# Optimization experiments

Measured on AMD Instinct MI355X. Metric: run time of the kernel, lower is better.

Reference implementation:

```python
import jax, jax.numpy as jnp
import numpy as np

D_MODEL = 1024
NUM_HEADS = 16
D_K = D_MODEL // NUM_HEADS


def setup_inputs() -> dict:
    key = jax.random.key(0)
    ks = jax.random.split(key, 7)
    B, S = 2, 2048
    query = jax.random.normal(ks[0], (B, S, D_MODEL), dtype=jnp.float32)
    key_t = jax.random.normal(ks[1], (B, S, D_MODEL), dtype=jnp.float32)
    value = jax.random.normal(ks[2], (B, S, D_MODEL), dtype=jnp.float32)
    attention_mask = jnp.ones((B, S), dtype=jnp.int32)
    # xavier_uniform for square d_model x d_model: limit = sqrt(6/(fan_in+fan_out))
    limit = np.sqrt(6.0 / (D_MODEL + D_MODEL)).astype(np.float32)
    def xav(k):
        return jax.random.uniform(k, (D_MODEL, D_MODEL), dtype=jnp.float32, minval=-limit, maxval=limit)
    return {
        "query": query, "key": key_t, "value": value,
        "attention_mask": attention_mask,
        "w_q": xav(ks[3]), "w_k": xav(ks[4]), "w_v": xav(ks[5]), "w_o": xav(ks[6]),
    }


def reference(query, key, value, attention_mask, w_q, w_k, w_v, w_o):
    B, S, _ = query.shape
    # torch Linear: x @ W.T  (weights stored [out, in])
    def proj(x, w):
        y = jnp.einsum('bsd,ed->bse', x, w)
        return y.reshape(B, S, NUM_HEADS, D_K).transpose(0, 2, 1, 3)  # [B,H,S,Dk]
    q = proj(query, w_q)
    k = proj(key, w_k)
    v = proj(value, w_v)
    scores = jnp.einsum('bhqd,bhkd->bhqk', q, k) / jnp.sqrt(jnp.float32(D_K))
    # mask [B,S] -> [B,1,1,S]; masked_fill where mask == 0
    mask = (attention_mask[:, None, None, :] == 0)
    scores = jnp.where(mask, jnp.float32(-1e9), scores)
    attn = jax.nn.softmax(scores, axis=-1)
    # dropout p=0.0 (eval) -> identity
    context = jnp.einsum('bhqk,bhkd->bhqd', attn, v)
    context = context.transpose(0, 2, 1, 3).reshape(B, S, D_MODEL)
    return jnp.einsum('bsd,ed->bse', context, w_o)
```

## Files before the change

### kernel.cpp

```cpp
#include <hip/hip_runtime.h>
#include <hip/hip_bf16.h>


typedef short short8  __attribute__((ext_vector_type(8)));
typedef short short4v __attribute__((ext_vector_type(4)));
typedef float f32x4   __attribute__((ext_vector_type(4)));

#define D_MODEL 1024
#define SEQ     2048
#define NHEAD   16
#define DKD     64
#define HSTR    (SEQ * DKD)
#define QSCALE  0.1803368801111204f
#define EXP2F(x) exp2f(x)

#define MFMA16(a, b, c) __builtin_amdgcn_mfma_f32_16x16x32_bf16((a), (b), (c), 0, 0, 0)

__device__ __forceinline__ ushort f2bf(float f) {
    __hip_bfloat16 h = __float2bfloat16(f);
    return __builtin_bit_cast(ushort, h);
}

__device__ __forceinline__ short8 frag128(const ushort* base, int row, int c0) {
    int cb = (c0 * 2) ^ ((row & 7) << 4);
    return *(const short8*)((const char*)base + row * 128 + cb);
}
__device__ __forceinline__ short8 frag256(const ushort* base, int row, int c0) {
    int cb = (c0 * 2) ^ ((row & 7) << 4);
    return *(const short8*)((const char*)base + row * 256 + cb);
}

__global__ __launch_bounds__(256) void cvt_w(
    const float* __restrict__ s0, const float* __restrict__ s1, const float* __restrict__ s2,
    ushort* __restrict__ dst)
{
    const int z = blockIdx.y;
    const float* s = (z == 0) ? s0 : ((z == 1) ? s1 : s2);
    ushort* d = dst + (size_t)z * 1048576;
    const int i = (blockIdx.x * 256 + threadIdx.x) * 8;
    f32x4 a = *(const f32x4*)(s + i);
    f32x4 b = *(const f32x4*)(s + i + 4);
    short8 o;
    #pragma unroll
    for (int u = 0; u < 4; ++u) { o[u] = (short)f2bf(a[u]); o[4 + u] = (short)f2bf(b[u]); }
    *(short8*)(d + i) = o;
}

template<int LAYOUT, int A_BF16>
__global__ __launch_bounds__(256, 3) void gemm_nt(
    const void* __restrict__ A0, const void* __restrict__ A1, const void* __restrict__ A2,
    const ushort* __restrict__ W0, const ushort* __restrict__ W1, const ushort* __restrict__ W2,
    void* __restrict__ O0, void* __restrict__ O1, void* __restrict__ O2)
{
    const int z = blockIdx.z;
    const void*   A = (z == 0) ? A0 : ((z == 1) ? A1 : A2);
    const ushort* W = (z == 0) ? W0 : ((z == 1) ? W1 : W2);
    void* O         = (z == 0) ? O0 : ((z == 1) ? O1 : O2);

    const int bm = blockIdx.x * 128;
    const int bn = blockIdx.y * 128;
    const int tid = threadIdx.x;
    const int w = tid >> 6, l = tid & 63;
    const int wr = w >> 1, wc = w & 1;

    __shared__ ushort sm[16384];

    f32x4 acc[4][4] = {};
    short8 areg[4], wreg[4];
    const int srow = tid >> 3;
    const int sc8  = (tid & 7) << 3;
    const int scb  = (sc8 * 2);

    #define GLOADT(t_) {                                                                    \
        _Pragma("unroll")                                                                   \
        for (int i = 0; i < 4; ++i) {                                                       \
            int row = i * 32 + srow;                                                        \
            if (A_BF16) {                                                                   \
                areg[i] = *(const short8*)((const ushort*)A + (size_t)(bm + row) * 1024 + (t_) * 64 + sc8); \
            } else {                                                                        \
                const float* ap = (const float*)A + (size_t)(bm + row) * 1024 + (t_) * 64 + sc8; \
                f32x4 x0 = *(const f32x4*)ap, x1 = *(const f32x4*)(ap + 4);                 \
                _Pragma("unroll")                                                           \
                for (int u = 0; u < 4; ++u) { areg[i][u] = (short)f2bf(x0[u]); areg[i][4 + u] = (short)f2bf(x1[u]); } \
            }                                                                               \
            wreg[i] = *(const short8*)(W + (size_t)(bn + row) * 1024 + (t_) * 64 + sc8);    \
        } }

    #define GWRITET() {                                                                     \
        _Pragma("unroll")                                                                   \
        for (int i = 0; i < 4; ++i) {                                                       \
            int row = i * 32 + srow;                                                        \
            int cb  = scb ^ ((row & 7) << 4);                                               \
            *(short8*)((char*)sm + row * 128 + cb) = areg[i];                               \
            *(short8*)((char*)(sm + 8192) + row * 128 + cb) = wreg[i];                      \
        } }

    GLOADT(0);
    #pragma unroll 1
    for (int t = 0; t < 16; ++t) {
        GWRITET();
        __syncthreads();
        if (t < 15) GLOADT(t + 1);

        #pragma unroll
        for (int kk = 0; kk < 2; ++kk) {
            const int c0 = kk * 32 + ((l >> 4) << 3);
            short8 af[4], bf[4];
            #pragma unroll
            for (int mi = 0; mi < 4; ++mi)
                af[mi] = frag128(sm, wr * 64 + mi * 16 + (l & 15), c0);
            #pragma unroll
            for (int ni = 0; ni < 4; ++ni)
                bf[ni] = frag128(sm + 8192, wc * 64 + ni * 16 + (l & 15), c0);
            #pragma unroll
            for (int mi = 0; mi < 4; ++mi)
                #pragma unroll
                for (int ni = 0; ni < 4; ++ni)
                    acc[mi][ni] = MFMA16(af[mi], bf[ni], acc[mi][ni]);
        }
        __syncthreads();
    }
    #undef GLOADT
    #undef GWRITET

    if (LAYOUT == 0 && z == 2) {
        #pragma unroll
        for (int mi = 0; mi < 4; ++mi) {
            #pragma unroll
            for (int ni = 0; ni < 4; ++ni) {
                int n_l = wc * 64 + ni * 16 + (l & 15);
                int m0  = wr * 64 + mi * 16 + ((l >> 4) << 2);
                short4v v4;
                #pragma unroll
                for (int j = 0; j < 4; ++j) v4[j] = (short)f2bf(acc[mi][ni][j]);
                *(short4v*)((char*)sm + n_l * 256 + ((m0 * 2) ^ ((n_l & 7) << 4))) = v4;
            }
        }
        __syncthreads();
        const int row = tid >> 1, half = tid & 1;
        const int n_g = bn + row;
        const int bb  = bm >> 11;
        ushort* Op = (ushort*)O + (size_t)(bb * NHEAD + (n_g >> 6)) * HSTR
                     + (size_t)(n_g & 63) * SEQ + (bm & 2047) + half * 64;
        #pragma unroll
        for (int u = 0; u < 8; ++u) {
            short8 c = *(const short8*)((char*)sm + row * 256
                        + (((half * 64 + u * 8) * 2) ^ ((row & 7) << 4)));
            *(short8*)(Op + u * 8) = c;
        }
        return;
    }

    const float sc = (LAYOUT == 0 && z == 0) ? QSCALE : 1.0f;
    #pragma unroll
    for (int mi = 0; mi < 4; ++mi) {
        #pragma unroll
        for (int ni = 0; ni < 4; ++ni) {
            #pragma unroll
            for (int j = 0; j < 4; ++j) {
                int m = bm + wr * 64 + mi * 16 + ((l >> 4) << 2) + j;
                int n = bn + wc * 64 + ni * 16 + (l & 15);
                if (LAYOUT == 0) {
                    int b = m >> 11, s = m & 2047, h = n >> 6, dk = n & 63;
                    ((ushort*)O)[(size_t)(b * NHEAD + h) * HSTR + s * DKD + dk] = f2bf(acc[mi][ni][j] * sc);
                } else {
                    ((float*)O)[(size_t)m * 1024 + n] = acc[mi][ni][j];
                }
            }
        }
    }
}

__global__ __launch_bounds__(512, 4) void attn_fwd(
    const ushort* __restrict__ Q, const ushort* __restrict__ K, const ushort* __restrict__ Vt,
    const int* __restrict__ mask, ushort* __restrict__ ctx)
{
    const int tid = threadIdx.x;
    const int w = tid >> 6, l = tid & 63;
    const int hi = l >> 4, lo = l & 15;
    const int id  = blockIdx.x;
    const int nid = (id & 7) * 64 + (id >> 3);
    const int bh  = nid >> 4;
    const int q0  = (nid & 15) * 128;
    const int b   = bh >> 4, h = bh & 15;

    __shared__ ushort sm[2][16384];
    __shared__ int mflag;

    if (tid == 0) mflag = 1;
    __syncthreads();
    {
        int4 m0 = ((const int4*)(mask + b * SEQ))[tid];
        if (!(m0.x && m0.y && m0.z && m0.w)) mflag = 0;
    }

    const ushort* Qh = Q  + (size_t)bh * HSTR;
    const ushort* Kh = K  + (size_t)bh * HSTR;
    const ushort* Vh = Vt + (size_t)bh * HSTR;

    short8 qf[2];
    #pragma unroll
    for (int kk = 0; kk < 2; ++kk)
        qf[kk] = *(const short8*)(Qh + (size_t)(q0 + w * 16 + lo) * DKD + kk * 32 + hi * 8);

    f32x4 acc_o[4] = {};
    float m_run = -INFINITY, l_run = 0.0f;

    const int kr = tid >> 3;
    const int kc = (tid & 7) << 3;
    const int vr = tid >> 4;
    const int vkpb = (tid & 15) << 4;

    short8  kreg[2];
    short4v vreg0[2], vreg1[2];

    #define LOADT(kt_) {                                                                   \
        _Pragma("unroll")                                                                  \
        for (int i = 0; i < 2; ++i)                                                        \
            kreg[i] = *(const short8*)(Kh + (size_t)((kt_) * 128 + i * 64 + kr) * DKD + kc); \
        _Pragma("unroll")                                                                  \
        for (int i = 0; i < 2; ++i) {                                                      \
            const ushort* vp = Vh + (size_t)(i * 32 + vr) * SEQ + (kt_) * 128 + ((tid >> 2) & 3) * 32 + (tid & 3) * 4; \
            vreg0[i] = *(const short4v*)(vp);                                              \
            vreg1[i] = *(const short4v*)(vp + 16); } }

    #define WRITET(buf_) {                                                                 \
        _Pragma("unroll")                                                                  \
        for (int i = 0; i < 2; ++i) {                                                      \
            int r = i * 64 + kr;                                                           \
            *(short8*)((char*)sm[buf_] + r * 128 + ((kc * 2) ^ ((r & 7) << 4))) = kreg[i]; } \
        _Pragma("unroll")                                                                  \
        for (int i = 0; i < 2; ++i) {                                                      \
            int r = i * 32 + vr;                                                           \
            char* p = (char*)(sm[buf_] + 8192) + r * 256 + (vkpb ^ ((r & 7) << 4));        \
            *(short4v*)(p)     = vreg0[i];                                                 \
            *(short4v*)(p + 8) = vreg1[i]; } }

    LOADT(0); WRITET(0);
    __syncthreads();
    const bool allones = (mflag != 0);
    const f32x4 zf = {};

    #define HALF(nb_) {                                                                    \
        f32x4* s = s4 + 4 * (nb_);                                                         \
        if (!allones) {                                                                    \
            const int* mrow = mask + b * SEQ + kt * 128 + (nb_) * 64 + hi * 4;             \
            _Pragma("unroll")                                                              \
            for (int ni = 0; ni < 4; ++ni) {                                               \
                int4 mv = *(const int4*)(mrow + ni * 16);                                  \
                s[ni][0] = mv.x ? s[ni][0] : -1e9f;                                        \
                s[ni][1] = mv.y ? s[ni][1] : -1e9f;                                        \
                s[ni][2] = mv.z ? s[ni][2] : -1e9f;                                        \
                s[ni][3] = mv.w ? s[ni][3] : -1e9f;                                        \
            }                                                                              \
        }                                                                                  \
        float t0 = fmaxf(fmaxf(s[0][0], s[0][1]), fmaxf(s[0][2], s[0][3]));                \
        float t1 = fmaxf(fmaxf(s[1][0], s[1][1]), fmaxf(s[1][2], s[1][3]));                \
        float t2 = fmaxf(fmaxf(s[2][0], s[2][1]), fmaxf(s[2][2], s[2][3]));                \
        float t3 = fmaxf(fmaxf(s[3][0], s[3][1]), fmaxf(s[3][2], s[3][3]));                \
        float t = fmaxf(fmaxf(t0, t1), fmaxf(t2, t3));                                     \
        t = fmaxf(t, __shfl_xor(t, 16));                                                   \
        t = fmaxf(t, __shfl_xor(t, 32));                                                   \
        if (!__all(t <= m_run + 8.0f)) {       \
            float mnew = fmaxf(m_run, t);                                                  \
            float c = EXP2F(m_run - mnew);                                                 \
            m_run = mnew;                                                                  \
            l_run *= c;                                                                    \
            float cj[4];                                                                   \
            _Pragma("unroll")                                                              \
            for (int j = 0; j < 4; ++j) cj[j] = __shfl(c, (l & 48) | (hi * 4 + j));        \
            _Pragma("unroll")                                                              \
            for (int ni = 0; ni < 4; ++ni)                                                 \
                _Pragma("unroll")                                                          \
                for (int j = 0; j < 4; ++j) acc_o[ni][j] *= cj[j];                         \
        }                                                                                  \
        float rsA = 0.0f;                                                                  \
        _Pragma("unroll")                                                                  \
        for (int ni = 0; ni < 4; ++ni) {                                                   \
            _Pragma("unroll")                                                              \
            for (int j = 0; j < 4; ++j) s[ni][j] = EXP2F(s[ni][j] - m_run);                \
            rsA += (s[ni][0] + s[ni][1]) + (s[ni][2] + s[ni][3]);                          \
        }                                                                                  \
        rsA += __shfl_xor(rsA, 16);                                                        \
        rsA += __shfl_xor(rsA, 32);                                                        \
        l_run += rsA;                                                                      \
        short8 pa[2];                                                                      \
        _Pragma("unroll")                                                                  \
        for (int kk = 0; kk < 2; ++kk) {                                                   \
            _Pragma("unroll")                                                              \
            for (int j = 0; j < 4; ++j) {                                                  \
                pa[kk][j]     = (short)f2bf(s[2 * kk][j]);                                 \
                pa[kk][4 + j] = (short)f2bf(s[2 * kk + 1][j]);                             \
            }                                                                              \
        }                                                                                  \
        __builtin_amdgcn_s_setprio(1);                                                     \
        _Pragma("unroll")                                                                  \
        for (int kk = 0; kk < 2; ++kk) {                                                   \
            const int c0 = ((nb_) * 2 + kk) * 32 + hi * 8;                                 \
            _Pragma("unroll")                                                              \
            for (int ni = 0; ni < 4; ++ni) {                                               \
                short8 vf = frag256(vb, ni * 16 + lo, c0);                                 \
                acc_o[ni] = MFMA16(pa[kk], vf, acc_o[ni]);                                 \
            }                                                                              \
        }                                                                                  \
        __builtin_amdgcn_s_setprio(0); }

    #pragma unroll 1
    for (int kt = 0; kt < 16; ++kt) {
        const int cur = kt & 1;
        const ushort* kb = sm[cur];
        const ushort* vb = sm[cur] + 8192;

        if (kt < 15) LOADT(kt + 1);

        f32x4 s4[8];
        __builtin_amdgcn_s_setprio(1);
        #pragma unroll
        for (int ni = 0; ni < 8; ++ni)
            s4[ni] = MFMA16(frag128(kb, ni * 16 + lo, hi * 8), qf[0], zf);
        #pragma unroll
        for (int ni = 0; ni < 8; ++ni)
            s4[ni] = MFMA16(frag128(kb, ni * 16 + lo, 32 + hi * 8), qf[1], s4[ni]);
        __builtin_amdgcn_s_setprio(0);

        HALF(0)
        if (kt < 15) WRITET(cur ^ 1);
        HALF(1)

        __syncthreads();
    }
    #undef HALF
    #undef LOADT
    #undef WRITET

    float inv = 1.0f / l_run;
    float invj[4];
    #pragma unroll
    for (int j = 0; j < 4; ++j)
        invj[j] = __shfl(inv, (l & 48) | (hi * 4 + j));
    #pragma unroll
    for (int ni = 0; ni < 4; ++ni)
        #pragma unroll
        for (int j = 0; j < 4; ++j) {
            int qg = q0 + w * 16 + hi * 4 + j;
            ctx[(size_t)(b * SEQ + qg) * D_MODEL + h * DKD + ni * 16 + lo] = f2bf(acc_o[ni][j] * invj[j]);
        }
}

__global__ void ws_sentinel(float* __restrict__ out, int n, float code) {
    int i = blockIdx.x * blockDim.x + threadIdx.x;
    if (i < n) out[i] = (i == 0) ? code : 0.0f;
}

extern "C" void kernel_launch(void* const* d_in, const int* in_sizes, int n_in,
                              void* d_out, int out_size, void* d_ws, size_t ws_size,
                              hipStream_t stream) {
    const float* q    = (const float*)d_in[0];
    const float* k    = (const float*)d_in[1];
    const float* v    = (const float*)d_in[2];
    const int*   mask = (const int*)d_in[3];
    const float* wq   = (const float*)d_in[4];
    const float* wk   = (const float*)d_in[5];
    const float* wv   = (const float*)d_in[6];
    const float* wo   = (const float*)d_in[7];
    float* out = (float*)d_out;

    if (ws_size < (size_t)33554432) {
        float code = 100.0f + (float)(ws_size >> 20);
        ws_sentinel<<<(out_size + 255) / 256, 256, 0, stream>>>(out, out_size, code);
        return;
    }

    ushort* ws = (ushort*)d_ws;
    ushort* Qb = ws;
    ushort* Kb = ws + 4194304;
    ushort* Vb = ws + 8388608;
    ushort* Cb = ws + 12582912;

    dim3 blk(256, 1, 1);
    cvt_w<<<dim3(512, 3), blk, 0, stream>>>(wq, wk, wv, Cb);
    gemm_nt<0, 0><<<dim3(32, 8, 3), blk, 0, stream>>>(
        q, k, v, Cb, Cb + 1048576, Cb + 2097152, Qb, Kb, Vb);
    attn_fwd<<<dim3(512, 1, 1), dim3(512, 1, 1), 0, stream>>>(Qb, Kb, Vb, mask, Cb);
    cvt_w<<<dim3(512, 1), blk, 0, stream>>>(wo, wo, wo, Qb);
    gemm_nt<1, 1><<<dim3(32, 8, 1), blk, 0, stream>>>(
        Cb, Cb, Cb, Qb, Qb, Qb, out, out, out);
}
```

Measured before the change: 136.2 us.

## Switch attention to 32x32 MFMA with split-KV wave groups and LDS merge

Rewrites the attention inner loop to use 32x32x16 bf16 MFMA tiles instead of 16x16x32. Each wave now owns 32 query rows, and the two wave groups each process half of every 128-key tile. The two partial softmax states are combined at the end through shared memory. The goal is to cut LDS fragment reads and issue overhead per MFMA, and to halve per-wave softmax work per tile, at the cost of an extra final merge, more accumulator registers, and a changed V staging layout.

```diff
diff --git a/kernel.cpp b/kernel.cpp
--- a/kernel.cpp
+++ b/kernel.cpp
@@ -5,6 +5,7 @@
 typedef short short8  __attribute__((ext_vector_type(8)));
 typedef short short4v __attribute__((ext_vector_type(4)));
 typedef float f32x4   __attribute__((ext_vector_type(4)));
+typedef float f32x16  __attribute__((ext_vector_type(16)));
 
 #define D_MODEL 1024
 #define SEQ     2048
@@ -15,6 +16,7 @@
 #define EXP2F(x) exp2f(x)
 
 #define MFMA16(a, b, c) __builtin_amdgcn_mfma_f32_16x16x32_bf16((a), (b), (c), 0, 0, 0)
+#define MFMA32(a, b, c) __builtin_amdgcn_mfma_f32_32x32x16_bf16((a), (b), (c), 0, 0, 0)
 
 __device__ __forceinline__ ushort f2bf(float f) {
     __hip_bfloat16 h = __float2bfloat16(f);
@@ -177,7 +179,8 @@
 {
     const int tid = threadIdx.x;
     const int w = tid >> 6, l = tid & 63;
-    const int hi = l >> 4, lo = l & 15;
+    const int l31 = l & 31, hi5 = l >> 5;
+    const int g = w >> 2, wq = w & 3;
     const int id  = blockIdx.x;
     const int nid = (id & 7) * 64 + (id >> 3);
     const int bh  = nid >> 4;
@@ -198,112 +201,43 @@
     const ushort* Kh = K  + (size_t)bh * HSTR;
     const ushort* Vh = Vt + (size_t)bh * HSTR;
 
-    short8 qf[2];
+    short8 qf[4];
     #pragma unroll
-    for (int kk = 0; kk < 2; ++kk)
-        qf[kk] = *(const short8*)(Qh + (size_t)(q0 + w * 16 + lo) * DKD + kk * 32 + hi * 8);
-
-    f32x4 acc_o[4] = {};
+    for (int kk = 0; kk < 4; ++kk)
+        qf[kk] = *(const short8*)(Qh + (size_t)(q0 + wq * 32 + l31) * DKD + kk * 16 + hi5 * 8);
+
+    f32x16 acc0 = {}, acc1 = {};
     float m_run = -INFINITY, l_run = 0.0f;
 
-    const int kr = tid >> 3;
-    const int kc = (tid & 7) << 3;
-    const int vr = tid >> 4;
-    const int vkpb = (tid & 15) << 4;
-
+    const int kr  = tid >> 3;
+    const int oct = tid & 7;
+    const int vq  = oct & 3, vhalf = oct >> 2;
+    const int kcb = oct << 4;
     short8  kreg[2];
-    short4v vreg0[2], vreg1[2];
+    short4v vreg[4];
 
     #define LOADT(kt_) {                                                                   \
-        _Pragma("unroll")                                                                  \
-        for (int i = 0; i < 2; ++i)                                                        \
-            kreg[i] = *(const short8*)(Kh + (size_t)((kt_) * 128 + i * 64 + kr) * DKD + kc); \
-        _Pragma("unroll")                                                                  \
-        for (int i = 0; i < 2; ++i) {                                                      \
-            const ushort* vp = Vh + (size_t)(i * 32 + vr) * SEQ + (kt_) * 128 + ((tid >> 2) & 3) * 32 + (tid & 3) * 4; \
-            vreg0[i] = *(const short4v*)(vp);                                              \
-            vreg1[i] = *(const short4v*)(vp + 16); } }
+        kreg[0] = *(const short8*)(Kh + (size_t)((kt_) * 128 + kr) * DKD + (oct << 3));    \
+        kreg[1] = *(const short8*)(Kh + (size_t)((kt_) * 128 + 64 + kr) * DKD + (oct << 3)); \
+        const ushort* vp = Vh + (size_t)kr * SEQ + (kt_) * 128 + vhalf * 64 + vq * 16;     \
+        vreg[0] = *(const short4v*)(vp);                                                   \
+        vreg[1] = *(const short4v*)(vp + 8);                                               \
+        vreg[2] = *(const short4v*)(vp + 4);                                               \
+        vreg[3] = *(const short4v*)(vp + 12); }
 
     #define WRITET(buf_) {                                                                 \
-        _Pragma("unroll")                                                                  \
-        for (int i = 0; i < 2; ++i) {                                                      \
-            int r = i * 64 + kr;                                                           \
-            *(short8*)((char*)sm[buf_] + r * 128 + ((kc * 2) ^ ((r & 7) << 4))) = kreg[i]; } \
-        _Pragma("unroll")                                                                  \
-        for (int i = 0; i < 2; ++i) {                                                      \
-            int r = i * 32 + vr;                                                           \
-            char* p = (char*)(sm[buf_] + 8192) + r * 256 + (vkpb ^ ((r & 7) << 4));        \
-            *(short4v*)(p)     = vreg0[i];                                                 \
-            *(short4v*)(p + 8) = vreg1[i]; } }
+        { int r = kr;      *(short8*)((char*)sm[buf_] + r * 128 + (kcb ^ ((r & 7) << 4))) = kreg[0]; } \
+        { int r = 64 + kr; *(short8*)((char*)sm[buf_] + r * 128 + (kcb ^ ((r & 7) << 4))) = kreg[1]; } \
+        { char* p = (char*)(sm[buf_] + 8192) + kr * 256;                                   \
+          int pb = (vhalf * 64 + vq * 16) * 2;                                             \
+          _Pragma("unroll")                                                                \
+          for (int u = 0; u < 4; ++u)                                                      \
+            *(short4v*)(p + ((pb + 8 * u) ^ ((kr & 7) << 4))) = vreg[u]; } }
 
     LOADT(0); WRITET(0);
     __syncthreads();
     const bool allones = (mflag != 0);
-    const f32x4 zf = {};
-
-    #define HALF(nb_) {                                                                    \
-        f32x4* s = s4 + 4 * (nb_);                                                         \
-        if (!allones) {                                                                    \
-            const int* mrow = mask + b * SEQ + kt * 128 + (nb_) * 64 + hi * 4;             \
-            _Pragma("unroll")                                                              \
-            for (int ni = 0; ni < 4; ++ni) {                                               \
-                int4 mv = *(const int4*)(mrow + ni * 16);                                  \
-                s[ni][0] = mv.x ? s[ni][0] : -1e9f;                                        \
-                s[ni][1] = mv.y ? s[ni][1] : -1e9f;                                        \
-                s[ni][2] = mv.z ? s[ni][2] : -1e9f;                                        \
-                s[ni][3] = mv.w ? s[ni][3] : -1e9f;                                        \
-            }                                                                              \
-        }                                                                                  \
-        float t0 = fmaxf(fmaxf(s[0][0], s[0][1]), fmaxf(s[0][2], s[0][3]));                \
-        float t1 = fmaxf(fmaxf(s[1][0], s[1][1]), fmaxf(s[1][2], s[1][3]));                \
-        float t2 = fmaxf(fmaxf(s[2][0], s[2][1]), fmaxf(s[2][2], s[2][3]));                \
-        float t3 = fmaxf(fmaxf(s[3][0], s[3][1]), fmaxf(s[3][2], s[3][3]));                \
-        float t = fmaxf(fmaxf(t0, t1), fmaxf(t2, t3));                                     \
-        t = fmaxf(t, __shfl_xor(t, 16));                                                   \
-        t = fmaxf(t, __shfl_xor(t, 32));                                                   \
-        if (!__all(t <= m_run + 8.0f)) {       \
-            float mnew = fmaxf(m_run, t);                                                  \
-            float c = EXP2F(m_run - mnew);                                                 \
-            m_run = mnew;                                                                  \
-            l_run *= c;                                                                    \
-            float cj[4];                                                                   \
-            _Pragma("unroll")                                                              \
-            for (int j = 0; j < 4; ++j) cj[j] = __shfl(c, (l & 48) | (hi * 4 + j));        \
-            _Pragma("unroll")                                                              \
-            for (int ni = 0; ni < 4; ++ni)                                                 \
-                _Pragma("unroll")                                                          \
-                for (int j = 0; j < 4; ++j) acc_o[ni][j] *= cj[j];                         \
-        }                                                                                  \
-        float rsA = 0.0f;                                                                  \
-        _Pragma("unroll")                                                                  \
-        for (int ni = 0; ni < 4; ++ni) {                                                   \
-            _Pragma("unroll")                                                              \
-            for (int j = 0; j < 4; ++j) s[ni][j] = EXP2F(s[ni][j] - m_run);                \
-            rsA += (s[ni][0] + s[ni][1]) + (s[ni][2] + s[ni][3]);                          \
-        }                                                                                  \
-        rsA += __shfl_xor(rsA, 16);                                                        \
-        rsA += __shfl_xor(rsA, 32);                                                        \
-        l_run += rsA;                                                                      \
-        short8 pa[2];                                                                      \
-        _Pragma("unroll")                                                                  \
-        for (int kk = 0; kk < 2; ++kk) {                                                   \
-            _Pragma("unroll")                                                              \
-            for (int j = 0; j < 4; ++j) {                                                  \
-                pa[kk][j]     = (short)f2bf(s[2 * kk][j]);                                 \
-                pa[kk][4 + j] = (short)f2bf(s[2 * kk + 1][j]);                             \
-            }                                                                              \
-        }                                                                                  \
-        __builtin_amdgcn_s_setprio(1);                                                     \
-        _Pragma("unroll")                                                                  \
-        for (int kk = 0; kk < 2; ++kk) {                                                   \
-            const int c0 = ((nb_) * 2 + kk) * 32 + hi * 8;                                 \
-            _Pragma("unroll")                                                              \
-            for (int ni = 0; ni < 4; ++ni) {                                               \
-                short8 vf = frag256(vb, ni * 16 + lo, c0);                                 \
-                acc_o[ni] = MFMA16(pa[kk], vf, acc_o[ni]);                                 \
-            }                                                                              \
-        }                                                                                  \
-        __builtin_amdgcn_s_setprio(0); }
+    const f32x16 zf = {};
 
     #pragma unroll 1
     for (int kt = 0; kt < 16; ++kt) {
@@ -313,38 +247,112 @@
 
         if (kt < 15) LOADT(kt + 1);
 
-        f32x4 s4[8];
+        f32x16 s4[2];
         __builtin_amdgcn_s_setprio(1);
         #pragma unroll
-        for (int ni = 0; ni < 8; ++ni)
-            s4[ni] = MFMA16(frag128(kb, ni * 16 + lo, hi * 8), qf[0], zf);
-        #pragma unroll
-        for (int ni = 0; ni < 8; ++ni)
-            s4[ni] = MFMA16(frag128(kb, ni * 16 + lo, 32 + hi * 8), qf[1], s4[ni]);
+        for (int t = 0; t < 2; ++t) {
+            s4[t] = MFMA32(frag128(kb, g * 64 + t * 32 + l31, hi5 * 8), qf[0], zf);
+            #pragma unroll
+            for (int kk = 1; kk < 4; ++kk)
+                s4[t] = MFMA32(frag128(kb, g * 64 + t * 32 + l31, kk * 16 + hi5 * 8), qf[kk], s4[t]);
+        }
         __builtin_amdgcn_s_setprio(0);
 
-        HALF(0)
+        if (!allones) {
+            const int* mrow = mask + b * SEQ + kt * 128 + g * 64 + 4 * hi5;
+            #pragma unroll
+            for (int t = 0; t < 2; ++t)
+                #pragma unroll
+                for (int r4 = 0; r4 < 4; ++r4) {
+                    int4 mv = *(const int4*)(mrow + (t * 4 + r4) * 8);
+                    s4[t][r4 * 4 + 0] = mv.x ? s4[t][r4 * 4 + 0] : -1e9f;
+                    s4[t][r4 * 4 + 1] = mv.y ? s4[t][r4 * 4 + 1] : -1e9f;
+                    s4[t][r4 * 4 + 2] = mv.z ? s4[t][r4 * 4 + 2] : -1e9f;
+                    s4[t][r4 * 4 + 3] = mv.w ? s4[t][r4 * 4 + 3] : -1e9f;
+                }
+        }
+
+        float tm = s4[0][0];
+        #pragma unroll
+        for (int i = 1; i < 16; ++i) tm = fmaxf(tm, s4[0][i]);
+        #pragma unroll
+        for (int i = 0; i < 16; ++i) tm = fmaxf(tm, s4[1][i]);
+        tm = fmaxf(tm, __shfl_xor(tm, 32));
+
+        if (!__all(tm <= m_run + 8.0f)) {
+            float mnew = fmaxf(m_run, tm);
+            float c = EXP2F(m_run - mnew);
+            m_run = mnew;
+            l_run *= c;
+            float cj[16];
+            #pragma unroll
+            for (int r = 0; r < 16; ++r)
+                cj[r] = __shfl(c, (l & 32) | ((r & 3) + 8 * (r >> 2) + 4 * hi5));
+            #pragma unroll
+            for (int r = 0; r < 16; ++r) { acc0[r] *= cj[r]; acc1[r] *= cj[r]; }
+        }
+
+        float rs = 0.0f;
+        #pragma unroll
+        for (int t = 0; t < 2; ++t)
+            #pragma unroll
+            for (int i = 0; i < 16; ++i) { s4[t][i] = EXP2F(s4[t][i] - m_run); rs += s4[t][i]; }
+        rs += __shfl_xor(rs, 32);
+        l_run += rs;
+
+        short8 pa[4];
+        #pragma unroll
+        for (int kk = 0; kk < 4; ++kk)
+            #pragma unroll
+            for (int s = 0; s < 8; ++s)
+                pa[kk][s] = (short)f2bf(s4[kk >> 1][8 * (kk & 1) + s]);
+
         if (kt < 15) WRITET(cur ^ 1);
-        HALF(1)
+
+        __builtin_amdgcn_s_setprio(1);
+        #pragma unroll
+        for (int kk = 0; kk < 4; ++kk) {
+            acc0 = MFMA32(pa[kk], frag256(vb, l31,      g * 64 + kk * 16 + hi5 * 8), acc0);
+            acc1 = MFMA32(pa[kk], frag256(vb, 32 + l31, g * 64 + kk * 16 + hi5 * 8), acc1);
+        }
+        __builtin_amdgcn_s_setprio(0);
 
         __syncthreads();
     }
-    #undef HALF
     #undef LOADT
     #undef WRITET
 
-    float inv = 1.0f / l_run;
-    float invj[4];
-    #pragma unroll
-    for (int j = 0; j < 4; ++j)
-        invj[j] = __shfl(inv, (l & 48) | (hi * 4 + j));
-    #pragma unroll
-    for (int ni = 0; ni < 4; ++ni)
-        #pragma unroll
-        for (int j = 0; j < 4; ++j) {
-            int qg = q0 + w * 16 + hi * 4 + j;
-            ctx[(size_t)(b * SEQ + qg) * D_MODEL + h * DKD + ni * 16 + lo] = f2bf(acc_o[ni][j] * invj[j]);
-        }
+    __syncthreads();
+    float* mls  = (float*)sm;
+    float* accs = (float*)sm + 512;
+    if (g == 1) {
+        float* mp = mls + (wq * 64 + l) * 2;
+        mp[0] = m_run; mp[1] = l_run;
+        float* ap = accs + (wq * 64 + l) * 32;
+        #pragma unroll
+        for (int r = 0; r < 16; ++r) { ap[r] = acc0[r]; ap[16 + r] = acc1[r]; }
+    }
+    __syncthreads();
+    if (g == 0) {
+        const float* mp = mls + (wq * 64 + l) * 2;
+        float mB = mp[0], lB = mp[1];
+        float ms = fmaxf(m_run, mB);
+        float cA = EXP2F(m_run - ms), cB = EXP2F(mB - ms);
+        float li = 1.0f / (cA * l_run + cB * lB);
+        float sA = cA * li, sB = cB * li;
+        const float* ap = accs + (wq * 64 + l) * 32;
+        #pragma unroll
+        for (int r = 0; r < 16; ++r) {
+            int qp = (r & 3) + 8 * (r >> 2) + 4 * hi5;
+            float sAr = __shfl(sA, (l & 32) | qp);
+            float sBr = __shfl(sB, (l & 32) | qp);
+            float v0 = sAr * acc0[r] + sBr * ap[r];
+            float v1 = sAr * acc1[r] + sBr * ap[16 + r];
+            int qg = q0 + wq * 32 + qp;
+            ctx[(size_t)(b * SEQ + qg) * D_MODEL + h * DKD + l31]      = f2bf(v0);
+            ctx[(size_t)(b * SEQ + qg) * D_MODEL + h * DKD + 32 + l31] = f2bf(v1);
+        }
+    }
 }
 
 __global__ void ws_sentinel(float* __restrict__ out, int n, float code) {
```

After: 156.9 us. +15.1%, slower.

## Load GEMM weight tiles directly into LDS with double-buffered global_load_lds

Applied to the files above, without the earlier changes.

The weight operand of the projection GEMM is now loaded straight from global memory into shared memory with global_load_lds, into a double-buffered LDS tile. The source column offset is pre-swizzled so the existing XOR layout is kept. This removes the register staging and LDS write instructions for W and cuts VGPR pressure. In exchange LDS use grows from 32KB to 48KB per block, which may lower occupancy against the launch_bounds target of 3. It also relies on the existing barrier ordering to make the asynchronous LDS writes visible.

```diff
diff --git a/kernel.cpp b/kernel.cpp
--- a/kernel.cpp
+++ b/kernel.cpp
@@ -15,6 +15,10 @@
 #define EXP2F(x) exp2f(x)
 
 #define MFMA16(a, b, c) __builtin_amdgcn_mfma_f32_16x16x32_bf16((a), (b), (c), 0, 0, 0)
+
+#define GLDS16(gp, lp) __builtin_amdgcn_global_load_lds( \
+    (const __attribute__((address_space(1))) void*)(gp), \
+    (__attribute__((address_space(3))) void*)(lp), 16, 0, 0)
 
 __device__ __forceinline__ ushort f2bf(float f) {
     __hip_bfloat16 h = __float2bfloat16(f);
@@ -63,15 +67,16 @@
     const int w = tid >> 6, l = tid & 63;
     const int wr = w >> 1, wc = w & 1;
 
-    __shared__ ushort sm[16384];
+    __shared__ ushort smA[8192];
+    __shared__ ushort smW[2][8192];
 
     f32x4 acc[4][4] = {};
-    short8 areg[4], wreg[4];
+    short8 areg[4];
     const int srow = tid >> 3;
     const int sc8  = (tid & 7) << 3;
     const int scb  = (sc8 * 2);
 
-    #define GLOADT(t_) {                                                                    \
+    #define GLOADA(t_) {                                                                    \
         _Pragma("unroll")                                                                   \
         for (int i = 0; i < 4; ++i) {                                                       \
             int row = i * 32 + srow;                                                        \
@@ -83,35 +88,46 @@
                 _Pragma("unroll")                                                           \
                 for (int u = 0; u < 4; ++u) { areg[i][u] = (short)f2bf(x0[u]); areg[i][4 + u] = (short)f2bf(x1[u]); } \
             }                                                                               \
-            wreg[i] = *(const short8*)(W + (size_t)(bn + row) * 1024 + (t_) * 64 + sc8);    \
         } }
 
-    #define GWRITET() {                                                                     \
+    #define GWRITEA() {                                                                     \
         _Pragma("unroll")                                                                   \
         for (int i = 0; i < 4; ++i) {                                                       \
             int row = i * 32 + srow;                                                        \
             int cb  = scb ^ ((row & 7) << 4);                                               \
-            *(short8*)((char*)sm + row * 128 + cb) = areg[i];                               \
-            *(short8*)((char*)(sm + 8192) + row * 128 + cb) = wreg[i];                      \
+            *(short8*)((char*)smA + row * 128 + cb) = areg[i];                              \
         } }
 
-    GLOADT(0);
+    #define GLDSW(t_, buf_) {                                                               \
+        _Pragma("unroll")                                                                   \
+        for (int i = 0; i < 4; ++i) {                                                       \
+            int flat = i * 256 + tid;                                                       \
+            int row  = flat >> 3;                                                           \
+            int pcb  = (flat & 7) << 4;                                                     \
+            int sc   = (pcb ^ ((row & 7) << 4)) >> 1;                                       \
+            GLDS16(W + (size_t)(bn + row) * 1024 + (t_) * 64 + sc,                          \
+                   &smW[buf_][(i * 4 + w) * 512]);                                          \
+        } }
+
+    GLOADA(0);
+    GLDSW(0, 0);
     #pragma unroll 1
     for (int t = 0; t < 16; ++t) {
-        GWRITET();
+        GWRITEA();
         __syncthreads();
-        if (t < 15) GLOADT(t + 1);
-
+        if (t < 15) { GLOADA(t + 1); GLDSW(t + 1, (t + 1) & 1); }
+
+        const ushort* wb = smW[t & 1];
         #pragma unroll
         for (int kk = 0; kk < 2; ++kk) {
             const int c0 = kk * 32 + ((l >> 4) << 3);
             short8 af[4], bf[4];
             #pragma unroll
             for (int mi = 0; mi < 4; ++mi)
-                af[mi] = frag128(sm, wr * 64 + mi * 16 + (l & 15), c0);
+                af[mi] = frag128(smA, wr * 64 + mi * 16 + (l & 15), c0);
             #pragma unroll
             for (int ni = 0; ni < 4; ++ni)
-                bf[ni] = frag128(sm + 8192, wc * 64 + ni * 16 + (l & 15), c0);
+                bf[ni] = frag128(wb, wc * 64 + ni * 16 + (l & 15), c0);
             #pragma unroll
             for (int mi = 0; mi < 4; ++mi)
                 #pragma unroll
@@ -120,10 +136,12 @@
         }
         __syncthreads();
     }
-    #undef GLOADT
-    #undef GWRITET
+    #undef GLOADA
+    #undef GWRITEA
+    #undef GLDSW
 
     if (LAYOUT == 0 && z == 2) {
+        ushort* tb = &smW[0][0];
         #pragma unroll
         for (int mi = 0; mi < 4; ++mi) {
             #pragma unroll
@@ -133,7 +151,7 @@
                 short4v v4;
                 #pragma unroll
                 for (int j = 0; j < 4; ++j) v4[j] = (short)f2bf(acc[mi][ni][j]);
-                *(short4v*)((char*)sm + n_l * 256 + ((m0 * 2) ^ ((n_l & 7) << 4))) = v4;
+                *(short4v*)((char*)tb + n_l * 256 + ((m0 * 2) ^ ((n_l & 7) << 4))) = v4;
             }
         }
         __syncthreads();
@@ -144,7 +162,7 @@
                      + (size_t)(n_g & 63) * SEQ + (bm & 2047) + half * 64;
         #pragma unroll
         for (int u = 0; u < 8; ++u) {
-            short8 c = *(const short8*)((char*)sm + row * 256
+            short8 c = *(const short8*)((char*)tb + row * 256
                         + (((half * 64 + u * 8) * 2) ^ ((row & 7) << 4)));
             *(short8*)(Op + u * 8) = c;
         }
```

Measured after the change: 139.3 us. 1.02x slower.

## Halve attention block threads so each wave handles two query row groups

Applied to the files above, without the earlier changes.

The attention kernel now runs 256 threads (4 waves) per block instead of 512, and each wave computes 32 query rows as two 16-row groups. Each K fragment and V fragment read from LDS is reused across two MFMAs, which halves the LDS reads per unit of work. The whole 128-key tile is now softmaxed at once rather than in two halves. In exchange, per-thread register use roughly doubles (scores, accumulators, prefetch registers), which can lower occupancy. The global-load work per thread also doubles.

```diff
diff --git a/kernel.cpp b/kernel.cpp
--- a/kernel.cpp
+++ b/kernel.cpp
@@ -171,7 +171,7 @@
     }
 }
 
-__global__ __launch_bounds__(512, 4) void attn_fwd(
+__global__ __launch_bounds__(256, 2) void attn_fwd(
     const ushort* __restrict__ Q, const ushort* __restrict__ K, const ushort* __restrict__ Vt,
     const int* __restrict__ mask, ushort* __restrict__ ctx)
 {
@@ -190,48 +190,52 @@
     if (tid == 0) mflag = 1;
     __syncthreads();
     {
-        int4 m0 = ((const int4*)(mask + b * SEQ))[tid];
-        if (!(m0.x && m0.y && m0.z && m0.w)) mflag = 0;
+        const int4* mp = ((const int4*)(mask + b * SEQ)) + tid;
+        int4 m0 = mp[0], m1 = mp[256];
+        if (!(m0.x && m0.y && m0.z && m0.w && m1.x && m1.y && m1.z && m1.w)) mflag = 0;
     }
 
     const ushort* Qh = Q  + (size_t)bh * HSTR;
     const ushort* Kh = K  + (size_t)bh * HSTR;
     const ushort* Vh = Vt + (size_t)bh * HSTR;
 
-    short8 qf[2];
+    short8 qf[2][2];
     #pragma unroll
-    for (int kk = 0; kk < 2; ++kk)
-        qf[kk] = *(const short8*)(Qh + (size_t)(q0 + w * 16 + lo) * DKD + kk * 32 + hi * 8);
-
-    f32x4 acc_o[4] = {};
-    float m_run = -INFINITY, l_run = 0.0f;
+    for (int g = 0; g < 2; ++g)
+        #pragma unroll
+        for (int kk = 0; kk < 2; ++kk)
+            qf[g][kk] = *(const short8*)(Qh + (size_t)(q0 + w * 32 + g * 16 + lo) * DKD
+                                         + kk * 32 + hi * 8);
+
+    f32x4 acc[2][4] = {};
+    float m_run[2] = {-INFINITY, -INFINITY}, l_run[2] = {0.0f, 0.0f};
 
     const int kr = tid >> 3;
     const int kc = (tid & 7) << 3;
     const int vr = tid >> 4;
     const int vkpb = (tid & 15) << 4;
 
-    short8  kreg[2];
-    short4v vreg0[2], vreg1[2];
+    short8  kreg[4];
+    short4v vreg0[4], vreg1[4];
 
     #define LOADT(kt_) {                                                                   \
         _Pragma("unroll")                                                                  \
-        for (int i = 0; i < 2; ++i)                                                        \
-            kreg[i] = *(const short8*)(Kh + (size_t)((kt_) * 128 + i * 64 + kr) * DKD + kc); \
-        _Pragma("unroll")                                                                  \
-        for (int i = 0; i < 2; ++i) {                                                      \
-            const ushort* vp = Vh + (size_t)(i * 32 + vr) * SEQ + (kt_) * 128 + ((tid >> 2) & 3) * 32 + (tid & 3) * 4; \
+        for (int i = 0; i < 4; ++i)                                                        \
+            kreg[i] = *(const short8*)(Kh + (size_t)((kt_) * 128 + i * 32 + kr) * DKD + kc); \
+        _Pragma("unroll")                                                                  \
+        for (int i = 0; i < 4; ++i) {                                                      \
+            const ushort* vp = Vh + (size_t)(i * 16 + vr) * SEQ + (kt_) * 128 + ((tid >> 2) & 3) * 32 + (tid & 3) * 4; \
             vreg0[i] = *(const short4v*)(vp);                                              \
             vreg1[i] = *(const short4v*)(vp + 16); } }
 
     #define WRITET(buf_) {                                                                 \
         _Pragma("unroll")                                                                  \
-        for (int i = 0; i < 2; ++i) {                                                      \
-            int r = i * 64 + kr;                                                           \
+        for (int i = 0; i < 4; ++i) {                                                      \
+            int r = i * 32 + kr;                                                           \
             *(short8*)((char*)sm[buf_] + r * 128 + ((kc * 2) ^ ((r & 7) << 4))) = kreg[i]; } \
         _Pragma("unroll")                                                                  \
-        for (int i = 0; i < 2; ++i) {                                                      \
-            int r = i * 32 + vr;                                                           \
+        for (int i = 0; i < 4; ++i) {                                                      \
+            int r = i * 16 + vr;                                                           \
             char* p = (char*)(sm[buf_] + 8192) + r * 256 + (vkpb ^ ((r & 7) << 4));        \
             *(short4v*)(p)     = vreg0[i];                                                 \
             *(short4v*)(p + 8) = vreg1[i]; } }
@@ -241,69 +245,57 @@
     const bool allones = (mflag != 0);
     const f32x4 zf = {};
 
-    #define HALF(nb_) {                                                                    \
-        f32x4* s = s4 + 4 * (nb_);                                                         \
+    #define SMG(g_) {                                                                      \
         if (!allones) {                                                                    \
-            const int* mrow = mask + b * SEQ + kt * 128 + (nb_) * 64 + hi * 4;             \
+            const int* mrow = mask + b * SEQ + kt * 128 + hi * 4;                          \
             _Pragma("unroll")                                                              \
-            for (int ni = 0; ni < 4; ++ni) {                                               \
+            for (int ni = 0; ni < 8; ++ni) {                                               \
                 int4 mv = *(const int4*)(mrow + ni * 16);                                  \
-                s[ni][0] = mv.x ? s[ni][0] : -1e9f;                                        \
-                s[ni][1] = mv.y ? s[ni][1] : -1e9f;                                        \
-                s[ni][2] = mv.z ? s[ni][2] : -1e9f;                                        \
-                s[ni][3] = mv.w ? s[ni][3] : -1e9f;                                        \
+                s4[g_][ni][0] = mv.x ? s4[g_][ni][0] : -1e9f;                              \
+                s4[g_][ni][1] = mv.y ? s4[g_][ni][1] : -1e9f;                              \
+                s4[g_][ni][2] = mv.z ? s4[g_][ni][2] : -1e9f;                              \
+                s4[g_][ni][3] = mv.w ? s4[g_][ni][3] : -1e9f;                              \
             }                                                                              \
         }                                                                                  \
-        float t0 = fmaxf(fmaxf(s[0][0], s[0][1]), fmaxf(s[0][2], s[0][3]));                \
-        float t1 = fmaxf(fmaxf(s[1][0], s[1][1]), fmaxf(s[1][2], s[1][3]));                \
-        float t2 = fmaxf(fmaxf(s[2][0], s[2][1]), fmaxf(s[2][2], s[2][3]));                \
-        float t3 = fmaxf(fmaxf(s[3][0], s[3][1]), fmaxf(s[3][2], s[3][3]));                \
-        float t = fmaxf(fmaxf(t0, t1), fmaxf(t2, t3));                                     \
+        float t = fmaxf(fmaxf(s4[g_][0][0], s4[g_][0][1]), fmaxf(s4[g_][0][2], s4[g_][0][3])); \
+        _Pragma("unroll")                                                                  \
+        for (int ni = 1; ni < 8; ++ni) {                                                   \
+            float tn = fmaxf(fmaxf(s4[g_][ni][0], s4[g_][ni][1]),                          \
+                             fmaxf(s4[g_][ni][2], s4[g_][ni][3]));                         \
+            t = fmaxf(t, tn);                                                              \
+        }                                                                                  \
         t = fmaxf(t, __shfl_xor(t, 16));                                                   \
         t = fmaxf(t, __shfl_xor(t, 32));                                                   \
-        if (!__all(t <= m_run + 8.0f)) {       \
-            float mnew = fmaxf(m_run, t);                                                  \
-            float c = EXP2F(m_run - mnew);                                                 \
-            m_run = mnew;                                                                  \
-            l_run *= c;                                                                    \
+        if (!__all(t <= m_run[g_] + 8.0f)) {                                               \
+            float mnew = fmaxf(m_run[g_], t);                                              \
+            float c = EXP2F(m_run[g_] - mnew);                                             \
+            m_run[g_] = mnew;                                                              \
+            l_run[g_] *= c;                                                                \
             float cj[4];                                                                   \
             _Pragma("unroll")                                                              \
             for (int j = 0; j < 4; ++j) cj[j] = __shfl(c, (l & 48) | (hi * 4 + j));        \
             _Pragma("unroll")                                                              \
             for (int ni = 0; ni < 4; ++ni)                                                 \
                 _Pragma("unroll")                                                          \
-                for (int j = 0; j < 4; ++j) acc_o[ni][j] *= cj[j];                         \
+                for (int j = 0; j < 4; ++j) acc[g_][ni][j] *= cj[j];                       \
         }                                                                                  \
-        float rsA = 0.0f;                                                                  \
-        _Pragma("unroll")                                                                  \
-        for (int ni = 0; ni < 4; ++ni) {                                                   \
+        float rs = 0.0f;                                                                   \
+        _Pragma("unroll")                                                                  \
+        for (int ni = 0; ni < 8; ++ni) {                                                   \
             _Pragma("unroll")                                                              \
-            for (int j = 0; j < 4; ++j) s[ni][j] = EXP2F(s[ni][j] - m_run);                \
-            rsA += (s[ni][0] + s[ni][1]) + (s[ni][2] + s[ni][3]);                          \
+            for (int j = 0; j < 4; ++j) s4[g_][ni][j] = EXP2F(s4[g_][ni][j] - m_run[g_]);  \
+            rs += (s4[g_][ni][0] + s4[g_][ni][1]) + (s4[g_][ni][2] + s4[g_][ni][3]);       \
         }                                                                                  \
-        rsA += __shfl_xor(rsA, 16);                                                        \
-        rsA += __shfl_xor(rsA, 32);                                                        \
-        l_run += rsA;                                                                      \
-        short8 pa[2];                                                                      \
-        _Pragma("unroll")                                                                  \
-        for (int kk = 0; kk < 2; ++kk) {                                                   \
+        rs += __shfl_xor(rs, 16);                                                          \
+        rs += __shfl_xor(rs, 32);                                                          \
+        l_run[g_] += rs;                                                                   \
+        _Pragma("unroll")                                                                  \
+        for (int kk = 0; kk < 4; ++kk)                                                     \
             _Pragma("unroll")                                                              \
             for (int j = 0; j < 4; ++j) {                                                  \
-                pa[kk][j]     = (short)f2bf(s[2 * kk][j]);                                 \
-                pa[kk][4 + j] = (short)f2bf(s[2 * kk + 1][j]);                             \
-            }                                                                              \
-        }                                                                                  \
-        __builtin_amdgcn_s_setprio(1);                                                     \
-        _Pragma("unroll")                                                                  \
-        for (int kk = 0; kk < 2; ++kk) {                                                   \
-            const int c0 = ((nb_) * 2 + kk) * 32 + hi * 8;                                 \
-            _Pragma("unroll")                                                              \
-            for (int ni = 0; ni < 4; ++ni) {                                               \
-                short8 vf = frag256(vb, ni * 16 + lo, c0);                                 \
-                acc_o[ni] = MFMA16(pa[kk], vf, acc_o[ni]);                                 \
-            }                                                                              \
-        }                                                                                  \
-        __builtin_amdgcn_s_setprio(0); }
+                pa[g_][kk][j]     = (short)f2bf(s4[g_][2 * kk][j]);                        \
+                pa[g_][kk][4 + j] = (short)f2bf(s4[g_][2 * kk + 1][j]);                    \
+            } }
 
     #pragma unroll 1
     for (int kt = 0; kt < 16; ++kt) {
@@ -313,38 +305,63 @@
 
         if (kt < 15) LOADT(kt + 1);
 
-        f32x4 s4[8];
+        f32x4 s4[2][8];
         __builtin_amdgcn_s_setprio(1);
         #pragma unroll
-        for (int ni = 0; ni < 8; ++ni)
-            s4[ni] = MFMA16(frag128(kb, ni * 16 + lo, hi * 8), qf[0], zf);
-        #pragma unroll
-        for (int ni = 0; ni < 8; ++ni)
-            s4[ni] = MFMA16(frag128(kb, ni * 16 + lo, 32 + hi * 8), qf[1], s4[ni]);
+        for (int ni = 0; ni < 8; ++ni) {
+            short8 kf = frag128(kb, ni * 16 + lo, hi * 8);
+            s4[0][ni] = MFMA16(kf, qf[0][0], zf);
+            s4[1][ni] = MFMA16(kf, qf[1][0], zf);
+        }
+        #pragma unroll
+        for (int ni = 0; ni < 8; ++ni) {
+            short8 kf = frag128(kb, ni * 16 + lo, 32 + hi * 8);
+            s4[0][ni] = MFMA16(kf, qf[0][1], s4[0][ni]);
+            s4[1][ni] = MFMA16(kf, qf[1][1], s4[1][ni]);
+        }
         __builtin_amdgcn_s_setprio(0);
 
-        HALF(0)
+        short8 pa[2][4];
+        SMG(0)
+        SMG(1)
+
         if (kt < 15) WRITET(cur ^ 1);
-        HALF(1)
+
+        __builtin_amdgcn_s_setprio(1);
+        #pragma unroll
+        for (int kk = 0; kk < 4; ++kk) {
+            const int c0 = kk * 32 + hi * 8;
+            #pragma unroll
+            for (int ni = 0; ni < 4; ++ni) {
+                short8 vf = frag256(vb, ni * 16 + lo, c0);
+                acc[0][ni] = MFMA16(pa[0][kk], vf, acc[0][ni]);
+                acc[1][ni] = MFMA16(pa[1][kk], vf, acc[1][ni]);
+            }
+        }
+        __builtin_amdgcn_s_setprio(0);
 
         __syncthreads();
     }
-    #undef HALF
+    #undef SMG
     #undef LOADT
     #undef WRITET
 
-    float inv = 1.0f / l_run;
-    float invj[4];
     #pragma unroll
-    for (int j = 0; j < 4; ++j)
-        invj[j] = __shfl(inv, (l & 48) | (hi * 4 + j));
-    #pragma unroll
-    for (int ni = 0; ni < 4; ++ni)
-        #pragma unroll
-        for (int j = 0; j < 4; ++j) {
-            int qg = q0 + w * 16 + hi * 4 + j;
-            ctx[(size_t)(b * SEQ + qg) * D_MODEL + h * DKD + ni * 16 + lo] = f2bf(acc_o[ni][j] * invj[j]);
-        }
+    for (int g = 0; g < 2; ++g) {
+        float inv = 1.0f / l_run[g];
+        float invj[4];
+        #pragma unroll
+        for (int j = 0; j < 4; ++j)
+            invj[j] = __shfl(inv, (l & 48) | (hi * 4 + j));
+        #pragma unroll
+        for (int ni = 0; ni < 4; ++ni)
+            #pragma unroll
+            for (int j = 0; j < 4; ++j) {
+                int qg = q0 + w * 32 + g * 16 + hi * 4 + j;
+                ctx[(size_t)(b * SEQ + qg) * D_MODEL + h * DKD + ni * 16 + lo] =
+                    f2bf(acc[g][ni][j] * invj[j]);
+            }
+    }
 }
 
 __global__ void ws_sentinel(float* __restrict__ out, int n, float code) {
@@ -381,7 +398,7 @@
     cvt_w<<<dim3(512, 3), blk, 0, stream>>>(wq, wk, wv, Cb);
     gemm_nt<0, 0><<<dim3(32, 8, 3), blk, 0, stream>>>(
         q, k, v, Cb, Cb + 1048576, Cb + 2097152, Qb, Kb, Vb);
-    attn_fwd<<<dim3(512, 1, 1), dim3(512, 1, 1), 0, stream>>>(Qb, Kb, Vb, mask, Cb);
+    attn_fwd<<<dim3(512, 1, 1), blk, 0, stream>>>(Qb, Kb, Vb, mask, Cb);
     cvt_w<<<dim3(512, 1), blk, 0, stream>>>(wo, wo, wo, Qb);
     gemm_nt<1, 1><<<dim3(32, 8, 1), blk, 0, stream>>>(
         Cb, Cb, Cb, Qb, Qb, Qb, out, out, out);
```

Measured after the change: 136.4 us. Within noise of the previous version (+0.2%).
